# Kernel tuning notes

Hardware: AMD Instinct MI355X
Metric: run time of the kernel (lower is better)

The kernel has to match this reference:

```python
import jax, jax.numpy as jnp
import numpy as np

STRIDE = 1
PAD = 1
K = 3  # kernel size


def setup_inputs() -> dict:
    key = jax.random.key(0)
    k1, k2, k3, k4 = jax.random.split(key, 4)
    B, C, H, W, O = 4, 256, 64, 64, 256
    x = jax.random.normal(k1, (B, C, H, W), jnp.float32)
    offset = jax.random.normal(k2, (B, 2 * K * K, H, W), jnp.float32)
    mask = jax.random.uniform(k3, (B, K * K, H, W), jnp.float32)
    # kaiming-ish scale for the conv weight
    weight = jax.random.normal(k4, (O, C, K, K), jnp.float32) / np.float32(np.sqrt(C * K * K))
    return {"x": x, "offset": offset, "mask": mask, "weight": weight}


def _deform_conv2d(x, offset, mask, weight, stride=STRIDE, pad=PAD):
    """Modulated deformable conv v2 (torchvision deform_conv2d semantics)."""
    B, C, H, W = x.shape
    O, _, Kh, Kw = weight.shape
    KK = Kh * Kw
    Ho = (H + 2 * pad - Kh) // stride + 1
    Wo = (W + 2 * pad - Kw) // stride + 1

    # offset layout: [B, 2*KK, Ho, Wo], pairs are (dy, dx) per kernel tap
    off = offset.reshape(B, KK, 2, Ho, Wo)
    dy, dx = off[:, :, 0], off[:, :, 1]  # [B, KK, Ho, Wo]

    ki = (jnp.arange(KK) // Kw).astype(x.dtype)  # kernel row per tap
    kj = (jnp.arange(KK) % Kw).astype(x.dtype)   # kernel col per tap
    base_y = (jnp.arange(Ho) * stride - pad).astype(x.dtype)
    base_x = (jnp.arange(Wo) * stride - pad).astype(x.dtype)

    # sampling positions [B, KK, Ho, Wo]
    py = base_y[None, None, :, None] + ki[None, :, None, None] + dy
    px = base_x[None, None, None, :] + kj[None, :, None, None] + dx

    y0 = jnp.floor(py)
    x0 = jnp.floor(px)
    wy = py - y0  # fractional weights
    wx = px - x0
    y0i = y0.astype(jnp.int32)
    x0i = x0.astype(jnp.int32)

    x_bhwc = jnp.transpose(x, (0, 2, 3, 1))  # [B, H, W, C] for gathers
    b_idx = jnp.arange(B)[:, None, None, None]

    def gather(yi, xi):
        # zero outside the image (zero-padding bilinear sampling)
        valid = (yi >= 0) & (yi < H) & (xi >= 0) & (xi < W)
        v = x_bhwc[b_idx, jnp.clip(yi, 0, H - 1), jnp.clip(xi, 0, W - 1)]  # [B,KK,Ho,Wo,C]
        return v * valid[..., None].astype(x.dtype)

    one = jnp.asarray(1, x.dtype)
    sampled = (gather(y0i, x0i) * ((one - wy) * (one - wx))[..., None]
               + gather(y0i, x0i + 1) * ((one - wy) * wx)[..., None]
               + gather(y0i + 1, x0i) * (wy * (one - wx))[..., None]
               + gather(y0i + 1, x0i + 1) * (wy * wx)[..., None])

    sampled = sampled * mask.reshape(B, KK, Ho, Wo)[..., None]  # modulation

    # weighted accumulation == implicit GEMM over (c, kk)
    return jnp.einsum('bkhwc,ock->bohw', sampled, weight.reshape(O, C, KK))


def reference(x, offset, mask, weight):
    return _deform_conv2d(x, offset, mask, weight)
```

## Files before the change

### kernel.cpp

```cpp
#include <hip/hip_runtime.h>
#include <hip/hip_bf16.h>

#define BN 4
#define CN 256
#define HN 64
#define WN 64
#define ON 256
#define KKN 9
#define HWN 4096
#define KDIM 2304
#define KC 288

using frag_ab = __attribute__((ext_vector_type(8))) short;
using frag_cd = __attribute__((ext_vector_type(4))) float;
using short4v = __attribute__((ext_vector_type(4))) short;

static __device__ inline short f2bf(float f) {
    union { float f; unsigned u; } v; v.f = f;
    unsigned r = v.u + 0x7fffu + ((v.u >> 16) & 1u);
    return (short)(r >> 16);
}
static __device__ inline float bf2f(short s) {
    union { unsigned u; float f; } v; v.u = ((unsigned)(unsigned short)s) << 16;
    return v.f;
}

__global__ __launch_bounds__(256) void prep_kernel(const float* __restrict__ x,
                                                   const float* __restrict__ wsrc,
                                                   short* __restrict__ xb16,
                                                   short* __restrict__ wtb) {
    int bidx = blockIdx.x;
    int tid  = threadIdx.x;
    if (bidx < 1024) {
        __shared__ float tile[64][65];
        int b   = bidx >> 8;
        int rem = bidx & 255;
        int c0  = (rem >> 6) * 64;
        int p0  = (rem & 63) * 64;
        int tp = tid & 63, tc = tid >> 6;
        for (int i = 0; i < 16; ++i) {
            int c = tc + i * 4;
            tile[c][tp] = x[(b * CN + c0 + c) * HWN + p0 + tp];
        }
        __syncthreads();
        int tcc = tid & 63, tpp = tid >> 6;
        for (int i = 0; i < 16; ++i) {
            int p = tpp + i * 4;
            xb16[(b * HWN + p0 + p) * CN + c0 + tcc] = f2bf(tile[tcc][p]);
        }
    } else {
        int chunk = (bidx - 1024) * 256 + tid;
        int ob  = chunk / (KC * 64);
        int rem = chunk - ob * (KC * 64);
        int kc  = rem >> 6;
        int row = rem & 63;
        int o   = ob * 64 + row;
        int kk  = kc >> 5;
        int oct = kc & 31;
        frag_ab v;
        #pragma unroll
        for (int e = 0; e < 8; ++e)
            v[e] = f2bf(wsrc[(o * CN + oct * 8 + e) * 9 + kk]);
        *(frag_ab*)&wtb[(size_t)chunk * 8] = v;
    }
}

__global__ __launch_bounds__(256, 2) void fused_kernel(const short* __restrict__ xb16,
                                                       const short* __restrict__ wtb,
                                                       const float* __restrict__ offs,
                                                       const float* __restrict__ maskp,
                                                       float* __restrict__ out) {
    __shared__ union {
        short Ab[2][8448];
        float outb[32 * 257];
    } sm;
    int tid = threadIdx.x;
    int m0  = blockIdx.x * 32;
    int b   = m0 >> 12;
    int h   = (m0 >> 6) & 63;
    int w0  = m0 & 63;
    int wv  = tid >> 6, lane = tid & 63;
    int q   = lane >> 4, r = lane & 15;
    int wbase = 33 * (lane >> 1) * 8 + (lane & 1) * 4;

    frag_cd acc[2][4];
    #pragma unroll
    for (int i = 0; i < 2; ++i)
        #pragma unroll
        for (int j = 0; j < 4; ++j)
            acc[i][j] = (frag_cd){0.f, 0.f, 0.f, 0.f};

    for (int kk = 0; kk < KKN; ++kk) {
        short* dst = sm.Ab[kk & 1];
        int ki = kk / 3, kj = kk - ki * 3;
        #pragma unroll
        for (int i = 0; i < 8; ++i) {
            int mloc = wv * 8 + i;
            int wc   = w0 + mloc;
            int obase = ((b * 18 + kk * 2) * 64 + h) * 64 + wc;
            float dy = offs[obase];
            float dx = offs[obase + HWN];
            float mv = maskp[((b * 9 + kk) * 64 + h) * 64 + wc];
            float py = (float)(h - 1 + ki) + dy;
            float px = (float)(wc - 1 + kj) + dx;
            float y0f = floorf(py), x0f = floorf(px);
            float wy = py - y0f, wx = px - x0f;
            int y0 = (int)y0f, x0 = (int)x0f;
            int   cb[4];
            float cw[4];
            #pragma unroll
            for (int cy = 0; cy < 2; ++cy)
                #pragma unroll
                for (int cx = 0; cx < 2; ++cx) {
                    int yy = y0 + cy, xx = x0 + cx;
                    bool valid = (yy >= 0 && yy < HN && xx >= 0 && xx < WN);
                    int yc = min(max(yy, 0), HN - 1);
                    int xc = min(max(xx, 0), WN - 1);
                    cb[cy * 2 + cx] = ((b * HN + yc) * WN + xc) * CN;
                    float wgt = (cy ? wy : 1.f - wy) * (cx ? wx : 1.f - wx) * mv;
                    cw[cy * 2 + cx] = valid ? wgt : 0.f;
                }
            short4v v[4];
            #pragma unroll
            for (int c = 0; c < 4; ++c)
                v[c] = *(const short4v*)&xb16[cb[c] + lane * 4];
            short4v res;
            #pragma unroll
            for (int e = 0; e < 4; e += 2) {
                float a0 = cw[0] * bf2f(v[0][e]) + cw[1] * bf2f(v[1][e])
                         + cw[2] * bf2f(v[2][e]) + cw[3] * bf2f(v[3][e]);
                float a1 = cw[0] * bf2f(v[0][e + 1]) + cw[1] * bf2f(v[1][e + 1])
                         + cw[2] * bf2f(v[2][e + 1]) + cw[3] * bf2f(v[3][e + 1]);
                __hip_bfloat162 p2 = __float22bfloat162_rn(make_float2(a0, a1));
                res[e]     = *(short*)&p2.x;
                res[e + 1] = *(short*)&p2.y;
            }
            *(short4v*)&dst[wbase + mloc * 8] = res;
        }
        __syncthreads();
        #pragma unroll
        for (int ks = 0; ks < 8; ++ks) {
            frag_ab af[2], bf[4];
            #pragma unroll
            for (int i = 0; i < 2; ++i)
                af[i] = *(const frag_ab*)
                    &dst[(33 * (ks * 4 + q) + i * 16 + r) * 8];
            #pragma unroll
            for (int j = 0; j < 4; ++j)
                bf[j] = *(const frag_ab*)
                    &wtb[(((size_t)wv * KC + kk * 32 + ks * 4 + q) * 64
                          + j * 16 + r) * 8];
            #pragma unroll
            for (int i = 0; i < 2; ++i)
                #pragma unroll
                for (int j = 0; j < 4; ++j)
                    acc[i][j] = __builtin_amdgcn_mfma_f32_16x16x32_bf16(
                        af[i], bf[j], acc[i][j], 0, 0, 0);
        }
    }
    __syncthreads();

    #pragma unroll
    for (int i = 0; i < 2; ++i)
        #pragma unroll
        for (int j = 0; j < 4; ++j) {
            int ml = i * 16 + q * 4;
            int ol = wv * 64 + j * 16 + r;
            sm.outb[(ml + 0) * 257 + ol] = acc[i][j][0];
            sm.outb[(ml + 1) * 257 + ol] = acc[i][j][1];
            sm.outb[(ml + 2) * 257 + ol] = acc[i][j][2];
            sm.outb[(ml + 3) * 257 + ol] = acc[i][j][3];
        }
    __syncthreads();
    {
        int ww = tid & 31;
        int og = tid >> 5;
        #pragma unroll
        for (int oo = 0; oo < 32; ++oo) {
            int o = oo * 8 + og;
            out[(((size_t)b * ON + o) * HN + h) * WN + w0 + ww] =
                sm.outb[ww * 257 + o];
        }
    }
}

extern "C" void kernel_launch(void* const* d_in, const int* in_sizes, int n_in,
                              void* d_out, int out_size, void* d_ws, size_t ws_size,
                              hipStream_t stream) {
    const float* x      = (const float*)d_in[0];
    const float* offset = (const float*)d_in[1];
    const float* mask   = (const float*)d_in[2];
    const float* weight = (const float*)d_in[3];
    float* out = (float*)d_out;

    short* xb16 = (short*)d_ws;
    short* wtb  = (short*)((char*)d_ws + 8388608);

    hipLaunchKernelGGL(prep_kernel,  dim3(1312), dim3(256), 0, stream,
                       x, weight, xb16, wtb);
    hipLaunchKernelGGL(fused_kernel, dim3(512),  dim3(256), 0, stream,
                       xb16, wtb, offset, mask, out);
}
```

Before: 137.0 us.

## Precompute bilinear sample descriptors in prep kernel and software-prefetch gathers

Moves the offset/mask to corner-index and weight computation into the prep kernel, which writes a per-(tap, pixel) descriptor table to the workspace. The fused kernel stages those descriptors in LDS and issues the gather loads for the next tap while the current tap's MFMAs run, using register staging buffers. It also raises wave priority around the MFMA block and simplifies the bf16 unpacking. This is meant to hide gather latency and take address arithmetic off the main loop. The cost is extra global traffic for the descriptor table, more LDS use and higher register pressure from the staged loads, which may reduce occupancy.

New measurement: 125.7 us. -8.3%, faster.

```diff
diff --git a/kernel.cpp b/kernel.cpp
--- a/kernel.cpp
+++ b/kernel.cpp
@@ -1,7 +1,6 @@
 #include <hip/hip_runtime.h>
 #include <hip/hip_bf16.h>
 
-#define BN 4
 #define CN 256
 #define HN 64
 #define WN 64
@@ -14,21 +13,24 @@
 using frag_ab = __attribute__((ext_vector_type(8))) short;
 using frag_cd = __attribute__((ext_vector_type(4))) float;
 using short4v = __attribute__((ext_vector_type(4))) short;
+using int4v   = __attribute__((ext_vector_type(4))) int;
+using float4v = __attribute__((ext_vector_type(4))) float;
+using float2v = __attribute__((ext_vector_type(2))) float;
+using uint2v  = __attribute__((ext_vector_type(2))) unsigned;
 
 static __device__ inline short f2bf(float f) {
     union { float f; unsigned u; } v; v.f = f;
     unsigned r = v.u + 0x7fffu + ((v.u >> 16) & 1u);
     return (short)(r >> 16);
 }
-static __device__ inline float bf2f(short s) {
-    union { unsigned u; float f; } v; v.u = ((unsigned)(unsigned short)s) << 16;
-    return v.f;
-}
 
 __global__ __launch_bounds__(256) void prep_kernel(const float* __restrict__ x,
                                                    const float* __restrict__ wsrc,
+                                                   const float* __restrict__ offs,
+                                                   const float* __restrict__ maskp,
                                                    short* __restrict__ xb16,
-                                                   short* __restrict__ wtb) {
+                                                   short* __restrict__ wtb,
+                                                   int* __restrict__ descg) {
     int bidx = blockIdx.x;
     int tid  = threadIdx.x;
     if (bidx < 1024) {
@@ -48,7 +50,7 @@
             int p = tpp + i * 4;
             xb16[(b * HWN + p0 + p) * CN + c0 + tcc] = f2bf(tile[tcc][p]);
         }
-    } else {
+    } else if (bidx < 1312) {
         int chunk = (bidx - 1024) * 256 + tid;
         int ob  = chunk / (KC * 64);
         int rem = chunk - ob * (KC * 64);
@@ -62,26 +64,69 @@
         for (int e = 0; e < 8; ++e)
             v[e] = f2bf(wsrc[(o * CN + oct * 8 + e) * 9 + kk]);
         *(frag_ab*)&wtb[(size_t)chunk * 8] = v;
+    } else {
+        int u  = (bidx - 1312) * 256 + tid;
+        int kk = u >> 14;
+        int m  = u & 16383;
+        int b  = m >> 12;
+        int p  = m & 4095;
+        int h  = p >> 6;
+        int w  = p & 63;
+        int ki = kk / 3, kj = kk - ki * 3;
+        float dy = offs[(b * 18 + 2 * kk) * HWN + p];
+        float dx = offs[(b * 18 + 2 * kk + 1) * HWN + p];
+        float mv = maskp[(b * 9 + kk) * HWN + p];
+        float py = (float)(h - 1 + ki) + dy;
+        float px = (float)(w - 1 + kj) + dx;
+        float y0f = floorf(py), x0f = floorf(px);
+        float wy = py - y0f, wx = px - x0f;
+        int y0 = (int)y0f, x0 = (int)x0f;
+        int4v cb; float4v cw;
+        #pragma unroll
+        for (int cy = 0; cy < 2; ++cy)
+            #pragma unroll
+            for (int cx = 0; cx < 2; ++cx) {
+                int yy = y0 + cy, xx = x0 + cx;
+                bool valid = (yy >= 0 && yy < HN && xx >= 0 && xx < WN);
+                int yc = min(max(yy, 0), HN - 1);
+                int xc = min(max(xx, 0), WN - 1);
+                cb[cy * 2 + cx] = ((b * HN + yc) * WN + xc) * CN;
+                float wgt = (cy ? wy : 1.f - wy) * (cx ? wx : 1.f - wx) * mv;
+                cw[cy * 2 + cx] = valid ? wgt : 0.f;
+            }
+        int* dd = descg + (size_t)u * 8;
+        *(int4v*)dd       = cb;
+        *(float4v*)(dd + 4) = cw;
     }
 }
 
 __global__ __launch_bounds__(256, 2) void fused_kernel(const short* __restrict__ xb16,
                                                        const short* __restrict__ wtb,
-                                                       const float* __restrict__ offs,
-                                                       const float* __restrict__ maskp,
+                                                       const int* __restrict__ descg,
                                                        float* __restrict__ out) {
-    __shared__ union {
-        short Ab[2][8448];
-        float outb[32 * 257];
+    __shared__ struct {
+        union {
+            short Ab[2][8448];
+            float outb[32 * 257];
+        } mix;
+        int desc[2304];
     } sm;
-    int tid = threadIdx.x;
-    int m0  = blockIdx.x * 32;
-    int b   = m0 >> 12;
-    int h   = (m0 >> 6) & 63;
-    int w0  = m0 & 63;
-    int wv  = tid >> 6, lane = tid & 63;
-    int q   = lane >> 4, r = lane & 15;
+    int tid  = threadIdx.x;
+    int m0   = blockIdx.x * 32;
+    int b    = m0 >> 12;
+    int h    = (m0 >> 6) & 63;
+    int w0   = m0 & 63;
+    int wv   = __builtin_amdgcn_readfirstlane(tid >> 6);
+    int lane = tid & 63;
+    int q    = lane >> 4, r = lane & 15;
     int wbase = 33 * (lane >> 1) * 8 + (lane & 1) * 4;
+    int lane4 = lane * 4;
+    int wv8   = wv * 8;
+
+    #pragma unroll
+    for (int kk = 0; kk < KKN; ++kk)
+        sm.desc[kk * 256 + tid] = descg[((size_t)kk * 16384 + m0) * 8 + tid];
+    __syncthreads();
 
     frag_cd acc[2][4];
     #pragma unroll
@@ -90,53 +135,48 @@
         for (int j = 0; j < 4; ++j)
             acc[i][j] = (frag_cd){0.f, 0.f, 0.f, 0.f};
 
+    short4v stg[8][4];
+    float4v cwc[8];
+
+    auto prefetch = [&](int kk1) {
+        #pragma unroll
+        for (int i = 0; i < 8; ++i) {
+            int dbase = (kk1 * 32 + wv8 + i) * 8;
+            int4v cb = *(const int4v*)&sm.desc[dbase];
+            cwc[i]   = *(const float4v*)&sm.desc[dbase + 4];
+            #pragma unroll
+            for (int c = 0; c < 4; ++c)
+                stg[i][c] = *(const short4v*)&xb16[cb[c] + lane4];
+        }
+    };
+
+    prefetch(0);
+
     for (int kk = 0; kk < KKN; ++kk) {
-        short* dst = sm.Ab[kk & 1];
-        int ki = kk / 3, kj = kk - ki * 3;
+        short* dst = sm.mix.Ab[kk & 1];
         #pragma unroll
         for (int i = 0; i < 8; ++i) {
-            int mloc = wv * 8 + i;
-            int wc   = w0 + mloc;
-            int obase = ((b * 18 + kk * 2) * 64 + h) * 64 + wc;
-            float dy = offs[obase];
-            float dx = offs[obase + HWN];
-            float mv = maskp[((b * 9 + kk) * 64 + h) * 64 + wc];
-            float py = (float)(h - 1 + ki) + dy;
-            float px = (float)(wc - 1 + kj) + dx;
-            float y0f = floorf(py), x0f = floorf(px);
-            float wy = py - y0f, wx = px - x0f;
-            int y0 = (int)y0f, x0 = (int)x0f;
-            int   cb[4];
-            float cw[4];
-            #pragma unroll
-            for (int cy = 0; cy < 2; ++cy)
+            float4v cw = cwc[i];
+            short4v res;
+            #pragma unroll
+            for (int g = 0; g < 2; ++g) {
+                float2v a = (float2v){0.f, 0.f};
                 #pragma unroll
-                for (int cx = 0; cx < 2; ++cx) {
-                    int yy = y0 + cy, xx = x0 + cx;
-                    bool valid = (yy >= 0 && yy < HN && xx >= 0 && xx < WN);
-                    int yc = min(max(yy, 0), HN - 1);
-                    int xc = min(max(xx, 0), WN - 1);
-                    cb[cy * 2 + cx] = ((b * HN + yc) * WN + xc) * CN;
-                    float wgt = (cy ? wy : 1.f - wy) * (cx ? wx : 1.f - wx) * mv;
-                    cw[cy * 2 + cx] = valid ? wgt : 0.f;
+                for (int c = 0; c < 4; ++c) {
+                    uint2v uv = __builtin_bit_cast(uint2v, stg[i][c]);
+                    unsigned uu = uv[g];
+                    float2v f;
+                    f.x = __builtin_bit_cast(float, uu << 16);
+                    f.y = __builtin_bit_cast(float, uu & 0xffff0000u);
+                    a += f * cw[c];
                 }
-            short4v v[4];
-            #pragma unroll
-            for (int c = 0; c < 4; ++c)
-                v[c] = *(const short4v*)&xb16[cb[c] + lane * 4];
-            short4v res;
-            #pragma unroll
-            for (int e = 0; e < 4; e += 2) {
-                float a0 = cw[0] * bf2f(v[0][e]) + cw[1] * bf2f(v[1][e])
-                         + cw[2] * bf2f(v[2][e]) + cw[3] * bf2f(v[3][e]);
-                float a1 = cw[0] * bf2f(v[0][e + 1]) + cw[1] * bf2f(v[1][e + 1])
-                         + cw[2] * bf2f(v[2][e + 1]) + cw[3] * bf2f(v[3][e + 1]);
-                __hip_bfloat162 p2 = __float22bfloat162_rn(make_float2(a0, a1));
-                res[e]     = *(short*)&p2.x;
-                res[e + 1] = *(short*)&p2.y;
+                __hip_bfloat162 p2 = __float22bfloat162_rn(make_float2(a.x, a.y));
+                res[2 * g]     = *(short*)&p2.x;
+                res[2 * g + 1] = *(short*)&p2.y;
             }
-            *(short4v*)&dst[wbase + mloc * 8] = res;
-        }
+            *(short4v*)&dst[wbase + (wv8 + i) * 8] = res;
+        }
+        if (kk < 8) prefetch(kk + 1);
         __syncthreads();
         #pragma unroll
         for (int ks = 0; ks < 8; ++ks) {
@@ -150,12 +190,14 @@
                 bf[j] = *(const frag_ab*)
                     &wtb[(((size_t)wv * KC + kk * 32 + ks * 4 + q) * 64
                           + j * 16 + r) * 8];
+            __builtin_amdgcn_s_setprio(1);
             #pragma unroll
             for (int i = 0; i < 2; ++i)
                 #pragma unroll
                 for (int j = 0; j < 4; ++j)
                     acc[i][j] = __builtin_amdgcn_mfma_f32_16x16x32_bf16(
                         af[i], bf[j], acc[i][j], 0, 0, 0);
+            __builtin_amdgcn_s_setprio(0);
         }
     }
     __syncthreads();
@@ -166,10 +208,10 @@
         for (int j = 0; j < 4; ++j) {
             int ml = i * 16 + q * 4;
             int ol = wv * 64 + j * 16 + r;
-            sm.outb[(ml + 0) * 257 + ol] = acc[i][j][0];
-            sm.outb[(ml + 1) * 257 + ol] = acc[i][j][1];
-            sm.outb[(ml + 2) * 257 + ol] = acc[i][j][2];
-            sm.outb[(ml + 3) * 257 + ol] = acc[i][j][3];
+            sm.mix.outb[(ml + 0) * 257 + ol] = acc[i][j][0];
+            sm.mix.outb[(ml + 1) * 257 + ol] = acc[i][j][1];
+            sm.mix.outb[(ml + 2) * 257 + ol] = acc[i][j][2];
+            sm.mix.outb[(ml + 3) * 257 + ol] = acc[i][j][3];
         }
     __syncthreads();
     {
@@ -179,7 +221,7 @@
         for (int oo = 0; oo < 32; ++oo) {
             int o = oo * 8 + og;
             out[(((size_t)b * ON + o) * HN + h) * WN + w0 + ww] =
-                sm.outb[ww * 257 + o];
+                sm.mix.outb[ww * 257 + o];
         }
     }
 }
@@ -193,11 +235,12 @@
     const float* weight = (const float*)d_in[3];
     float* out = (float*)d_out;
 
-    short* xb16 = (short*)d_ws;
-    short* wtb  = (short*)((char*)d_ws + 8388608);
-
-    hipLaunchKernelGGL(prep_kernel,  dim3(1312), dim3(256), 0, stream,
-                       x, weight, xb16, wtb);
+    short* xb16  = (short*)d_ws;
+    short* wtb   = (short*)((char*)d_ws + 8388608);
+    int*   descg = (int*)((char*)d_ws + 9568256);
+
+    hipLaunchKernelGGL(prep_kernel,  dim3(1888), dim3(256), 0, stream,
+                       x, weight, offset, mask, xb16, wtb, descg);
     hipLaunchKernelGGL(fused_kernel, dim3(512),  dim3(256), 0, stream,
-                       xb16, wtb, offset, mask, out);
-}
+                       xb16, wtb, descg, out);
+}
```
